# Kernel tuning notes

Measured on AMD Instinct MI355X. Metric: run time of the kernel, lower is better.

The kernel has to match this reference:

```python
import jax, jax.numpy as jnp
import numpy as np

D_MODEL = 1024
NUM_HEADS = 16
D_K = D_MODEL // NUM_HEADS  # 64


def _xavier(key, shape):
    fan_in, fan_out = shape[-1], shape[-2]
    limit = float(np.sqrt(6.0 / (fan_in + fan_out)))
    return jax.random.uniform(key, shape, jnp.float32, -limit, limit)


def setup_inputs() -> dict:
    key = jax.random.key(0)
    kx, kq, kk, kv, ko = jax.random.split(key, 5)
    x = jax.random.normal(kx, (2, 2048, D_MODEL), dtype=jnp.float32)
    q_heads = _xavier(kq, (NUM_HEADS, D_K, D_MODEL))
    k_heads = _xavier(kk, (NUM_HEADS, D_K, D_MODEL))
    v_heads = _xavier(kv, (NUM_HEADS, D_K, D_MODEL))
    output_proj = _xavier(ko, (D_MODEL, NUM_HEADS * D_K))
    return {"x": x, "q_heads": q_heads, "k_heads": k_heads,
            "v_heads": v_heads, "output_proj": output_proj}


def reference(x, q_heads, k_heads, v_heads, output_proj):
    # x: [b, s, d]; q/k/v_heads: [h, dk, d]; output_proj: [d, h*dk]
    b, s, d = x.shape
    h, dk, _ = q_heads.shape
    scale = 1.0 / jnp.sqrt(jnp.asarray(dk, x.dtype))
    # per-head projections: [b, h, s, dk]
    Q = jnp.einsum('bsd,hkd->bhsk', x, q_heads)
    K = jnp.einsum('bsd,hkd->bhsk', x, k_heads)
    V = jnp.einsum('bsd,hkd->bhsk', x, v_heads)
    scores = jnp.einsum('bhqk,bhsk->bhqs', Q, K) * scale  # [b,h,s,s]
    causal = jnp.tril(jnp.ones((s, s), dtype=bool))       # True where allowed
    scores = jnp.where(causal, scores, -jnp.inf)
    attn = jax.nn.softmax(scores, axis=-1)
    out = jnp.einsum('bhqs,bhsk->bhqk', attn, V)           # [b,h,s,dk]
    out = out.transpose(0, 2, 1, 3).reshape(b, s, h * dk)  # [b,s,h*dk]
    return jnp.einsum('bsk,dk->bsd', out, output_proj)
```

## Files before the change

kernel.cpp:

```cpp
#include <hip/hip_runtime.h>
#include <hip/hip_bf16.h>
#include <math.h>

#define D_MODEL 1024
#define NHEADS  16
#define DK      64
#define SEQ     2048
#define KDIM    1024

typedef __bf16 bf16x8 __attribute__((ext_vector_type(8)));
typedef float  f32x4  __attribute__((ext_vector_type(4)));

__device__ __forceinline__ void gload16(const void* g, void* l) {
    __builtin_amdgcn_global_load_lds(
        (const __attribute__((address_space(1))) void*)g,
        (__attribute__((address_space(3))) void*)l, 16, 0, 0);
}

__device__ __forceinline__ unsigned short f2bf(float f) {
    __hip_bfloat16 h = __float2bfloat16(f);
    return *(unsigned short*)&h;
}

__device__ __forceinline__ unsigned pk2bf(float a, float b) {
    __hip_bfloat162 h = __float22bfloat162_rn(make_float2(a, b));
    return *(unsigned*)&h;
}

#define QSCALE 0.18033688011112042f

__global__ __launch_bounds__(256) void cast_kernel(
    const float* __restrict__ x,
    const float* __restrict__ qw,
    const float* __restrict__ kw,
    const float* __restrict__ vw,
    const float* __restrict__ wo,
    unsigned short* __restrict__ xb,
    unsigned short* __restrict__ wqkv,
    unsigned short* __restrict__ wob)
{
    const size_t t = (size_t)blockIdx.x * 256 + threadIdx.x;
    const size_t X4 = 1048576;
    const size_t W4 = 262144;

    const float* src;
    unsigned short* dst;
    size_t o;
    if (t < X4)            { src = x;  dst = xb;             o = t; }
    else if (t < X4 + W4)  { src = qw; dst = wqkv;           o = t - X4; }
    else if (t < X4 + 2*W4){ src = kw; dst = wqkv + 1048576; o = t - X4 - W4; }
    else if (t < X4 + 3*W4){ src = vw; dst = wqkv + 2097152; o = t - X4 - 2*W4; }
    else                   { src = wo; dst = wob;            o = t - X4 - 3*W4; }

    float4 v = ((const float4*)src)[o];
    ushort4 r;
    r.x = f2bf(v.x); r.y = f2bf(v.y); r.z = f2bf(v.z); r.w = f2bf(v.w);
    ((ushort4*)dst)[o] = r;
}

template<int MODE>
__global__ __launch_bounds__(256) void mfma_gemm(
    const unsigned short* __restrict__ A,
    const unsigned short* __restrict__ B,
    float* __restrict__ C0,
    unsigned short* __restrict__ Qb,
    unsigned short* __restrict__ Kb,
    unsigned short* __restrict__ Vtb)
{
    __shared__ unsigned short As[128 * 32];
    __shared__ unsigned short Bs[128 * 32];

    const int tid  = threadIdx.x;
    const int wave = tid >> 6;
    const int lane = tid & 63;
    const int wr   = wave >> 1;
    const int wc   = wave & 1;
    const int quad = lane >> 4;
    const int l16  = lane & 15;

    const int rowBase = blockIdx.y * 128;
    const int colBase = blockIdx.x * 128;

    f32x4 acc[4][4];
    const f32x4 z = {0.f, 0.f, 0.f, 0.f};
#pragma unroll
    for (int i = 0; i < 4; ++i)
#pragma unroll
        for (int j = 0; j < 4; ++j) acc[i][j] = z;

    const int srow = lane >> 2;
    const int skof = (lane & 3) * 8;

    for (int k0 = 0; k0 < KDIM; k0 += 32) {
        __syncthreads();

        const unsigned short* ga =
            A + (size_t)(rowBase + wave * 32) * KDIM + k0;
        gload16(ga + (size_t)srow * KDIM + skof,        &As[(wave*32)    * 32]);
        gload16(ga + (size_t)(16 + srow) * KDIM + skof, &As[(wave*32+16) * 32]);

        const unsigned short* gb =
            B + (size_t)(colBase + wave * 32) * KDIM + k0;
        gload16(gb + (size_t)srow * KDIM + skof,        &Bs[(wave*32)    * 32]);
        gload16(gb + (size_t)(16 + srow) * KDIM + skof, &Bs[(wave*32+16) * 32]);

        __syncthreads();

        bf16x8 af[4], bfr[4];
#pragma unroll
        for (int t = 0; t < 4; ++t)
            af[t] = *(const bf16x8*)&As[(wr*64 + t*16 + l16) * 32 + quad*8];
#pragma unroll
        for (int t = 0; t < 4; ++t)
            bfr[t] = *(const bf16x8*)&Bs[(wc*64 + t*16 + l16) * 32 + quad*8];

#pragma unroll
        for (int tr = 0; tr < 4; ++tr)
#pragma unroll
            for (int tc = 0; tc < 4; ++tc)
                acc[tr][tc] = __builtin_amdgcn_mfma_f32_16x16x32_bf16(
                    af[tr], bfr[tc], acc[tr][tc], 0, 0, 0);
    }

#pragma unroll
    for (int tr = 0; tr < 4; ++tr) {
#pragma unroll
        for (int tc = 0; tc < 4; ++tc) {
            const int grow0 = rowBase + wr*64 + tr*16 + quad*4;
            const int gcol  = colBase + wc*64 + tc*16 + l16;
            if (MODE == 0) {
                const int m  = gcol >> 10;
                const int kk = gcol & 1023;
                const int h  = kk >> 6, dk = kk & 63;
                const int b  = grow0 >> 11, s0 = grow0 & (SEQ - 1);
                if (m == 2) {
                    ushort4 pk;
                    pk.x = f2bf(acc[tr][tc][0]); pk.y = f2bf(acc[tr][tc][1]);
                    pk.z = f2bf(acc[tr][tc][2]); pk.w = f2bf(acc[tr][tc][3]);
                    *(ushort4*)(Vtb + ((size_t)(b*NHEADS + h)*DK + dk)*SEQ + s0) = pk;
                } else {
                    unsigned short* dst = (m == 0 ? Qb : Kb);
                    const float sc = (m == 0) ? QSCALE : 1.0f;
#pragma unroll
                    for (int reg = 0; reg < 4; ++reg)
                        dst[((size_t)(b*NHEADS + h)*SEQ + s0 + reg)*DK + dk] =
                            f2bf(acc[tr][tc][reg] * sc);
                }
            } else {
#pragma unroll
                for (int reg = 0; reg < 4; ++reg)
                    C0[(size_t)(grow0 + reg) * D_MODEL + gcol] = acc[tr][tc][reg];
            }
        }
    }
}

__global__ __launch_bounds__(256) void attn_mfma_kernel(
    const unsigned short* __restrict__ Qb,
    const unsigned short* __restrict__ Kb,
    const unsigned short* __restrict__ Vtb,
    unsigned short* __restrict__ O)
{
    __shared__ unsigned short Ks[64 * 64];
    __shared__ unsigned short Vs[64 * 64];
    __shared__ unsigned short Ps[4 * 16 * 64];

    const int bh   = blockIdx.x;
    const int qt   = 31 - blockIdx.y;
    const int wave = threadIdx.x >> 6;
    const int lane = threadIdx.x & 63;
    const int quad = lane >> 4;
    const int l16  = lane & 15;

    const size_t qrow = (size_t)bh * SEQ + qt*64 + wave*16 + l16;
    bf16x8 aq0 = *(const bf16x8*)(Qb + qrow * DK + quad*8);
    bf16x8 aq1 = *(const bf16x8*)(Qb + qrow * DK + 32 + quad*8);

    f32x4 o_acc[4];
    const f32x4 z = {0.f, 0.f, 0.f, 0.f};
#pragma unroll
    for (int i = 0; i < 4; ++i) o_acc[i] = z;
    float lrow = 0.f;

    const int srow8  = lane >> 3;
    const int schunk = lane & 7;
    const unsigned short* Kbase = Kb  + (size_t)bh * SEQ * DK;
    const unsigned short* Vbase = Vtb + (size_t)bh * DK * SEQ;
    unsigned short* Pw = &Ps[wave * 1024];

    const int ntiles = qt + 1;
    for (int jt = 0; jt < ntiles; ++jt) {
        const int j0 = jt * 64;
        __syncthreads();
#pragma unroll
        for (int n = 0; n < 2; ++n) {
            const int r = wave*16 + n*8 + srow8;
            gload16(Kbase + (size_t)(j0 + r) * DK + (schunk ^ srow8) * 8,
                    &Ks[(wave*16 + n*8) * 64]);
            gload16(Vbase + (size_t)r * SEQ + j0 + (schunk ^ srow8) * 8,
                    &Vs[(wave*16 + n*8) * 64]);
        }
        __syncthreads();

        f32x4 st[4];
#pragma unroll
        for (int ct = 0; ct < 4; ++ct) {
            const int r = ct*16 + l16;
            bf16x8 k0 = *(const bf16x8*)&Ks[r*64 + ((quad     ^ (r&7)) * 8)];
            bf16x8 k1 = *(const bf16x8*)&Ks[r*64 + (((4+quad) ^ (r&7)) * 8)];
            f32x4 t = z;
            t = __builtin_amdgcn_mfma_f32_16x16x32_bf16(k0, aq0, t, 0, 0, 0);
            t = __builtin_amdgcn_mfma_f32_16x16x32_bf16(k1, aq1, t, 0, 0, 0);
            st[ct] = t;
        }

        if (jt == qt) {
#pragma unroll
            for (int ct = 0; ct < 4; ++ct)
#pragma unroll
                for (int reg = 0; reg < 4; ++reg) {
                    const int kl = ct*16 + quad*4 + reg;
                    const int ql = wave*16 + l16;
                    if (kl > ql) st[ct][reg] = -1e30f;
                }
        }

        float rs = 0.f;
#pragma unroll
        for (int ct = 0; ct < 4; ++ct)
#pragma unroll
            for (int reg = 0; reg < 4; ++reg) {
                float p = exp2f(st[ct][reg]);
                st[ct][reg] = p;
                rs += p;
            }
        rs += __shfl_xor(rs, 16);
        rs += __shfl_xor(rs, 32);
        lrow += rs;

#pragma unroll
        for (int ct = 0; ct < 4; ++ct) {
            uint2 pk;
            pk.x = pk2bf(st[ct][0], st[ct][1]);
            pk.y = pk2bf(st[ct][2], st[ct][3]);
            const int g = (ct*4 + quad) ^ ((l16 & 7) << 1);
            *(uint2*)(Pw + l16*64 + g*4) = pk;
        }

        bf16x8 bp0 = *(const bf16x8*)(Pw + l16*64 + ((quad     ^ (l16&7)) * 8));
        bf16x8 bp1 = *(const bf16x8*)(Pw + l16*64 + (((4+quad) ^ (l16&7)) * 8));

#pragma unroll
        for (int ot = 0; ot < 4; ++ot) {
            const int r = ot*16 + l16;
            bf16x8 v0 = *(const bf16x8*)&Vs[r*64 + ((quad     ^ (r&7)) * 8)];
            bf16x8 v1 = *(const bf16x8*)&Vs[r*64 + (((4+quad) ^ (r&7)) * 8)];
            o_acc[ot] = __builtin_amdgcn_mfma_f32_16x16x32_bf16(v0, bp0, o_acc[ot], 0, 0, 0);
            o_acc[ot] = __builtin_amdgcn_mfma_f32_16x16x32_bf16(v1, bp1, o_acc[ot], 0, 0, 0);
        }
    }

    const float inv = 1.f / lrow;
    const int b = bh >> 4, h = bh & 15;
    const int sg = qt*64 + wave*16 + l16;
    unsigned short* orow = O + ((size_t)(b * SEQ + sg)) * D_MODEL + h * DK;
#pragma unroll
    for (int ot = 0; ot < 4; ++ot) {
        uint2 pk;
        pk.x = pk2bf(o_acc[ot][0] * inv, o_acc[ot][1] * inv);
        pk.y = pk2bf(o_acc[ot][2] * inv, o_acc[ot][3] * inv);
        *(uint2*)(orow + ot*16 + quad*4) = pk;
    }
}

extern "C" void kernel_launch(void* const* d_in, const int* in_sizes, int n_in,
                              void* d_out, int out_size, void* d_ws, size_t ws_size,
                              hipStream_t stream) {
    const float* x  = (const float*)d_in[0];
    const float* qw = (const float*)d_in[1];
    const float* kw = (const float*)d_in[2];
    const float* vw = (const float*)d_in[3];
    const float* wo = (const float*)d_in[4];
    float* out = (float*)d_out;

    char* ws = (char*)d_ws;
    unsigned short* Qb   = (unsigned short*)(ws);
    unsigned short* Kb   = (unsigned short*)(ws + (size_t) 8*1024*1024);
    unsigned short* Vtb  = (unsigned short*)(ws + (size_t)16*1024*1024);
    unsigned short* AO   = (unsigned short*)(ws + (size_t)24*1024*1024);
    unsigned short* XB   = (unsigned short*)(ws + (size_t)32*1024*1024);
    unsigned short* WQKV = (unsigned short*)(ws + (size_t)40*1024*1024);
    unsigned short* WOB  = (unsigned short*)(ws + (size_t)46*1024*1024);

    cast_kernel<<<8192, 256, 0, stream>>>(x, qw, kw, vw, wo, XB, WQKV, WOB);

    dim3 g1(24, 32);
    mfma_gemm<0><<<g1, 256, 0, stream>>>(XB, WQKV, nullptr, Qb, Kb, Vtb);

    dim3 g2(32, 32);
    attn_mfma_kernel<<<g2, 256, 0, stream>>>(Qb, Kb, Vtb, AO);

    dim3 g3(8, 32);
    mfma_gemm<1><<<g3, 256, 0, stream>>>(AO, WOB, out, nullptr, nullptr, nullptr);
}
```

Measured before the change: 186.5 us.

## Split key dimension across waves in causal attention with LDS reduction

Result: slower. 218.7 us (+17.3%).

```diff
diff --git a/kernel.cpp b/kernel.cpp
--- a/kernel.cpp
+++ b/kernel.cpp
@@ -161,9 +161,10 @@
     const unsigned short* __restrict__ Vtb,
     unsigned short* __restrict__ O)
 {
-    __shared__ unsigned short Ks[64 * 64];
-    __shared__ unsigned short Vs[64 * 64];
-    __shared__ unsigned short Ps[4 * 16 * 64];
+    __shared__ __align__(16) unsigned short smem[24576];
+    unsigned short* Ks = smem;
+    unsigned short* Vs = smem + 8192;
+    unsigned short* Ps = smem + 16384;
 
     const int bh   = blockIdx.x;
     const int qt   = 31 - blockIdx.y;
@@ -171,106 +172,174 @@
     const int lane = threadIdx.x & 63;
     const int quad = lane >> 4;
     const int l16  = lane & 15;
-
-    const size_t qrow = (size_t)bh * SEQ + qt*64 + wave*16 + l16;
-    bf16x8 aq0 = *(const bf16x8*)(Qb + qrow * DK + quad*8);
-    bf16x8 aq1 = *(const bf16x8*)(Qb + qrow * DK + 32 + quad*8);
-
-    f32x4 o_acc[4];
+    const int q0   = qt * 64;
+    const int kw0  = wave * 32;
+
+    bf16x8 qf[4][2];
+#pragma unroll
+    for (int qs = 0; qs < 4; ++qs) {
+        const size_t qrow = (size_t)bh * SEQ + q0 + qs*16 + l16;
+        qf[qs][0] = *(const bf16x8*)(Qb + qrow * DK + quad*8);
+        qf[qs][1] = *(const bf16x8*)(Qb + qrow * DK + 32 + quad*8);
+    }
+
     const f32x4 z = {0.f, 0.f, 0.f, 0.f};
-#pragma unroll
-    for (int i = 0; i < 4; ++i) o_acc[i] = z;
-    float lrow = 0.f;
-
-    const int srow8  = lane >> 3;
-    const int schunk = lane & 7;
+    f32x4 o_acc[4][4];
+#pragma unroll
+    for (int i = 0; i < 4; ++i)
+#pragma unroll
+        for (int j = 0; j < 4; ++j) o_acc[i][j] = z;
+    float lsum[4] = {0.f, 0.f, 0.f, 0.f};
+
     const unsigned short* Kbase = Kb  + (size_t)bh * SEQ * DK;
     const unsigned short* Vbase = Vtb + (size_t)bh * DK * SEQ;
-    unsigned short* Pw = &Ps[wave * 1024];
-
-    const int ntiles = qt + 1;
-    for (int jt = 0; jt < ntiles; ++jt) {
-        const int j0 = jt * 64;
+    unsigned short* Pw = Ps + wave * 2048;
+
+    const int srow8 = lane >> 3, schunk = lane & 7;
+    const int vrow4 = lane >> 4, vpos   = lane & 15;
+
+    const int R = (qt + 2) >> 1;
+    for (int jt = 0; jt < R; ++jt) {
+        const int j0 = jt << 7;
         __syncthreads();
 #pragma unroll
-        for (int n = 0; n < 2; ++n) {
-            const int r = wave*16 + n*8 + srow8;
-            gload16(Kbase + (size_t)(j0 + r) * DK + (schunk ^ srow8) * 8,
-                    &Ks[(wave*16 + n*8) * 64]);
-            gload16(Vbase + (size_t)r * SEQ + j0 + (schunk ^ srow8) * 8,
-                    &Vs[(wave*16 + n*8) * 64]);
+        for (int n = 0; n < 4; ++n) {
+            const int r = wave*32 + n*8 + srow8;
+            gload16(Kbase + (size_t)(j0 + r) * DK + ((schunk ^ srow8) << 3),
+                    Ks + (wave*32 + n*8) * 64);
+        }
+#pragma unroll
+        for (int n = 0; n < 4; ++n) {
+            const int r = wave*16 + n*4 + vrow4;
+            gload16(Vbase + (size_t)r * SEQ + j0 + ((vpos ^ (r & 7)) << 3),
+                    Vs + (wave*16 + n*4) * 128);
         }
         __syncthreads();
 
-        f32x4 st[4];
-#pragma unroll
-        for (int ct = 0; ct < 4; ++ct) {
-            const int r = ct*16 + l16;
-            bf16x8 k0 = *(const bf16x8*)&Ks[r*64 + ((quad     ^ (r&7)) * 8)];
-            bf16x8 k1 = *(const bf16x8*)&Ks[r*64 + (((4+quad) ^ (r&7)) * 8)];
-            f32x4 t = z;
-            t = __builtin_amdgcn_mfma_f32_16x16x32_bf16(k0, aq0, t, 0, 0, 0);
-            t = __builtin_amdgcn_mfma_f32_16x16x32_bf16(k1, aq1, t, 0, 0, 0);
-            st[ct] = t;
+        if (j0 + kw0 <= q0 + 63) {
+            f32x4 st[2][4];
+#pragma unroll
+            for (int ks = 0; ks < 2; ++ks) {
+                const int row = kw0 + ks*16 + l16;
+                bf16x8 k0 = *(const bf16x8*)&Ks[row*64 + (((    quad) ^ (row & 7)) << 3)];
+                bf16x8 k1 = *(const bf16x8*)&Ks[row*64 + (((4 + quad) ^ (row & 7)) << 3)];
+#pragma unroll
+                for (int qs = 0; qs < 4; ++qs) {
+                    f32x4 t = z;
+                    t = __builtin_amdgcn_mfma_f32_16x16x32_bf16(k0, qf[qs][0], t, 0, 0, 0);
+                    t = __builtin_amdgcn_mfma_f32_16x16x32_bf16(k1, qf[qs][1], t, 0, 0, 0);
+                    st[ks][qs] = t;
+                }
+            }
+
+            if (j0 + kw0 + 31 > q0) {
+#pragma unroll
+                for (int ks = 0; ks < 2; ++ks)
+#pragma unroll
+                    for (int qs = 0; qs < 4; ++qs)
+#pragma unroll
+                        for (int reg = 0; reg < 4; ++reg) {
+                            const int kg = j0 + kw0 + ks*16 + quad*4 + reg;
+                            const int qg = q0 + qs*16 + l16;
+                            if (kg > qg) st[ks][qs][reg] = -1e30f;
+                        }
+            }
+
+#pragma unroll
+            for (int qs = 0; qs < 4; ++qs) {
+                float rs = 0.f;
+#pragma unroll
+                for (int ks = 0; ks < 2; ++ks)
+#pragma unroll
+                    for (int reg = 0; reg < 4; ++reg) {
+                        float p = exp2f(st[ks][qs][reg]);
+                        st[ks][qs][reg] = p;
+                        rs += p;
+                    }
+                rs += __shfl_xor(rs, 16);
+                rs += __shfl_xor(rs, 32);
+                lsum[qs] += rs;
+
+                const int row = qs*16 + l16;
+#pragma unroll
+                for (int ks = 0; ks < 2; ++ks) {
+                    uint2 pk;
+                    pk.x = pk2bf(st[ks][qs][0], st[ks][qs][1]);
+                    pk.y = pk2bf(st[ks][qs][2], st[ks][qs][3]);
+                    const int g = (ks*4 + quad) ^ ((row & 3) << 1);
+                    *(uint2*)(Pw + row*32 + g*4) = pk;
+                }
+            }
+
+            bf16x8 pf[4];
+#pragma unroll
+            for (int qs = 0; qs < 4; ++qs) {
+                const int row = qs*16 + l16;
+                pf[qs] = *(const bf16x8*)&Pw[row*32 + ((quad ^ (row & 3)) << 3)];
+            }
+#pragma unroll
+            for (int ot = 0; ot < 4; ++ot) {
+                const int row = ot*16 + l16;
+                bf16x8 vf = *(const bf16x8*)&Vs[row*128 +
+                                (((wave*4 + quad) ^ (row & 7)) << 3)];
+#pragma unroll
+                for (int qs = 0; qs < 4; ++qs)
+                    o_acc[ot][qs] = __builtin_amdgcn_mfma_f32_16x16x32_bf16(
+                        vf, pf[qs], o_acc[ot][qs], 0, 0, 0);
+            }
         }
-
-        if (jt == qt) {
-#pragma unroll
-            for (int ct = 0; ct < 4; ++ct)
-#pragma unroll
-                for (int reg = 0; reg < 4; ++reg) {
-                    const int kl = ct*16 + quad*4 + reg;
-                    const int ql = wave*16 + l16;
-                    if (kl > ql) st[ct][reg] = -1e30f;
-                }
-        }
-
-        float rs = 0.f;
-#pragma unroll
-        for (int ct = 0; ct < 4; ++ct)
-#pragma unroll
-            for (int reg = 0; reg < 4; ++reg) {
-                float p = exp2f(st[ct][reg]);
-                st[ct][reg] = p;
-                rs += p;
-            }
-        rs += __shfl_xor(rs, 16);
-        rs += __shfl_xor(rs, 32);
-        lrow += rs;
-
-#pragma unroll
-        for (int ct = 0; ct < 4; ++ct) {
-            uint2 pk;
-            pk.x = pk2bf(st[ct][0], st[ct][1]);
-            pk.y = pk2bf(st[ct][2], st[ct][3]);
-            const int g = (ct*4 + quad) ^ ((l16 & 7) << 1);
-            *(uint2*)(Pw + l16*64 + g*4) = pk;
-        }
-
-        bf16x8 bp0 = *(const bf16x8*)(Pw + l16*64 + ((quad     ^ (l16&7)) * 8));
-        bf16x8 bp1 = *(const bf16x8*)(Pw + l16*64 + (((4+quad) ^ (l16&7)) * 8));
-
-#pragma unroll
-        for (int ot = 0; ot < 4; ++ot) {
-            const int r = ot*16 + l16;
-            bf16x8 v0 = *(const bf16x8*)&Vs[r*64 + ((quad     ^ (r&7)) * 8)];
-            bf16x8 v1 = *(const bf16x8*)&Vs[r*64 + (((4+quad) ^ (r&7)) * 8)];
-            o_acc[ot] = __builtin_amdgcn_mfma_f32_16x16x32_bf16(v0, bp0, o_acc[ot], 0, 0, 0);
-            o_acc[ot] = __builtin_amdgcn_mfma_f32_16x16x32_bf16(v1, bp1, o_acc[ot], 0, 0, 0);
-        }
-    }
-
-    const float inv = 1.f / lrow;
+    }
+
+    __syncthreads();
+    float* Am = (float*)smem;
+    float* Bm = (float*)(smem + 8192);
+    float* sl = (float*)(smem + 16384);
+
+    if (quad == 0) {
+#pragma unroll
+        for (int qs = 0; qs < 4; ++qs)
+            sl[wave*64 + qs*16 + l16] = lsum[qs];
+    }
+    float* dst = (wave & 1) ? Bm : Am;
+    if (wave < 2) {
+#pragma unroll
+        for (int ot = 0; ot < 4; ++ot)
+#pragma unroll
+            for (int qs = 0; qs < 4; ++qs)
+                *(f32x4*)&dst[(ot*4 + qs)*256 + lane*4] = o_acc[ot][qs];
+    }
+    __syncthreads();
+    if (wave >= 2) {
+#pragma unroll
+        for (int ot = 0; ot < 4; ++ot)
+#pragma unroll
+            for (int qs = 0; qs < 4; ++qs) {
+                f32x4* p = (f32x4*)&dst[(ot*4 + qs)*256 + lane*4];
+                *p = *p + o_acc[ot][qs];
+            }
+    }
+    __syncthreads();
+
+    const int tq  = threadIdx.x >> 2;
+    const int tot = threadIdx.x & 3;
+    const int qs  = tq >> 4, ql = tq & 15;
+    const float l_tot = sl[tq] + sl[64 + tq] + sl[128 + tq] + sl[192 + tq];
+    const float inv = 1.f / l_tot;
     const int b = bh >> 4, h = bh & 15;
-    const int sg = qt*64 + wave*16 + l16;
-    unsigned short* orow = O + ((size_t)(b * SEQ + sg)) * D_MODEL + h * DK;
-#pragma unroll
-    for (int ot = 0; ot < 4; ++ot) {
-        uint2 pk;
-        pk.x = pk2bf(o_acc[ot][0] * inv, o_acc[ot][1] * inv);
-        pk.y = pk2bf(o_acc[ot][2] * inv, o_acc[ot][3] * inv);
-        *(uint2*)(orow + ot*16 + quad*4) = pk;
-    }
+    unsigned short* orow = O + (size_t)(b * SEQ + q0 + tq) * D_MODEL
+                             + h * DK + tot * 16;
+    uint out8[8];
+#pragma unroll
+    for (int qd = 0; qd < 4; ++qd) {
+        const int off = (tot*4 + qs)*256 + (qd*16 + ql)*4;
+        f32x4 v = *(f32x4*)&Am[off];
+        f32x4 w = *(f32x4*)&Bm[off];
+        v = v + w;
+        out8[qd*2 + 0] = pk2bf(v[0] * inv, v[1] * inv);
+        out8[qd*2 + 1] = pk2bf(v[2] * inv, v[3] * inv);
+    }
+    *(uint4*)(orow)     = *(uint4*)&out8[0];
+    *(uint4*)(orow + 8) = *(uint4*)&out8[4];
 }
 
 extern "C" void kernel_launch(void* const* d_in, const int* in_sizes, int n_in,
```
